# Performance work log

Hardware: AMD Instinct MI355X
Metric: run time of the kernel (lower is better)

Reference implementation:

```python
import jax, jax.numpy as jnp
import numpy as np

B, S, IN, H, NC, WSEG = 2, 256, 80, 128, 40, 64
F2 = 2 * H  # bidirectional LSTM output dim


def setup_inputs() -> dict:
    key = jax.random.key(0)
    it = iter(jax.random.split(key, 48))
    def nrm(shape, scale):
        return jax.random.normal(next(it), shape, jnp.float32) * scale
    d = {}
    d["x"] = jax.random.normal(next(it), (B, S, IN), jnp.float32)
    d["lengths"] = jnp.full((B,), S, dtype=jnp.int32)
    ins = [IN, F2]
    for l in range(2):
        for dr in ("f", "b"):
            sc = 1.0 / np.sqrt(H)
            d[f"w_ih_l{l}{dr}"] = nrm((4 * H, ins[l]), sc)
            d[f"w_hh_l{l}{dr}"] = nrm((4 * H, H), sc)
            d[f"b_l{l}{dr}"] = nrm((4 * H,), sc)
    PD = 3 * F2  # pairwise phi feature dim
    d["a_s0"] = jnp.float32(0.25); d["w_s1"] = nrm((100, PD), 1.0 / np.sqrt(PD)); d["b_s1"] = jnp.zeros((100,), jnp.float32)
    d["a_s1"] = jnp.float32(0.25); d["w_s2"] = nrm((1, 100), 0.1); d["b_s2"] = jnp.zeros((1,), jnp.float32)
    d["a_c0"] = jnp.float32(0.25); d["w_c1"] = nrm((2 * NC, F2), 1.0 / np.sqrt(F2)); d["b_c1"] = jnp.zeros((2 * NC,), jnp.float32)
    d["a_c1"] = jnp.float32(0.25); d["w_c2"] = nrm((NC, 2 * NC), 0.1); d["b_c2"] = jnp.zeros((NC,), jnp.float32)
    d["a_b0"] = jnp.float32(0.25); d["w_b1"] = nrm((2 * NC, F2), 1.0 / np.sqrt(F2)); d["b_b1"] = jnp.zeros((2 * NC,), jnp.float32)
    d["a_b1"] = jnp.float32(0.25); d["w_b2"] = nrm((2, 2 * NC), 0.1); d["b_b2"] = jnp.zeros((2,), jnp.float32)
    return d


def prelu(x, a):
    return jnp.where(x >= 0, x, a * x)


def mlp(x, a0, W1, b1, a1, W2, b2):
    h = prelu(x, a0) @ W1.T + b1
    return prelu(h, a1) @ W2.T + b2


def lstm_dir(x, Wih, Whh, b, reverse):
    # PyTorch gate order: i, f, g, o
    pre = jnp.einsum("bsi,gi->sbg", x, Wih) + b  # [S,B,4H]
    if reverse:
        pre = pre[::-1]
    h0 = jnp.zeros((x.shape[0], Whh.shape[1]), x.dtype)
    def step(carry, xt):
        h, c = carry
        g = xt + h @ Whh.T
        i, f, gg, o = jnp.split(g, 4, axis=-1)
        c = jax.nn.sigmoid(f) * c + jax.nn.sigmoid(i) * jnp.tanh(gg)
        h = jax.nn.sigmoid(o) * jnp.tanh(c)
        return (h, c), h
    _, hs = jax.lax.scan(step, (h0, h0), pre)
    if reverse:
        hs = hs[::-1]
    return jnp.swapaxes(hs, 0, 1)  # [B,S,H]


def encode(x, layers):
    out = x
    for (wif, whf, bf, wib, whb, bb) in layers:
        out = jnp.concatenate([
            lstm_dir(out, wif, whf, bf, False),
            lstm_dir(out, wib, whb, bb, True),
        ], axis=-1)
    return out


def compute_scores(rnn_out, a_s0, w_s1, b_s1, a_s1, w_s2, b_s2):
    cum = jnp.cumsum(rnn_out, axis=1)
    # phi[b,i,j] = [cum[j]-cum[i], out[i], out[j]]  (faithful to calc_phi)
    c = cum[:, None, :, :] - cum[:, :, None, :]
    sh = c.shape
    dmat = jnp.broadcast_to(rnn_out[:, :, None, :], sh)
    emat = jnp.broadcast_to(rnn_out[:, None, :, :], sh)
    phi = jnp.concatenate([c, dmat, emat], axis=-1)  # [B,S,S,3*F2]
    return mlp(phi, a_s0, w_s1, b_s1, a_s1, w_s2, b_s2)[..., 0]  # [B,S,S]


def dp_backptr(scores):
    # Viterbi-style DP: best[i] = max_{j in [i-WSEG, i)} best[j] + scores[:, j, i]
    Bn, Sn = scores.shape[:2]
    def step(best, i):
        start = jnp.maximum(0, i - WSEG)
        jidx = start + jnp.arange(WSEG)
        bwin = jax.lax.dynamic_slice(best, (0, start), (Bn, WSEG))
        swin = jax.lax.dynamic_slice(scores, (0, start, i), (Bn, WSEG, 1))[..., 0]
        cand = jnp.where(jidx[None, :] < i, bwin + swin, -1e9)
        k = (start + jnp.argmax(cand, axis=1)).astype(jnp.int32)
        best = jax.lax.dynamic_update_slice(best, jnp.max(cand, axis=1, keepdims=True), (0, i))
        return best, k
    _, ks = jax.lax.scan(step, jnp.zeros((Bn, Sn), scores.dtype), jnp.arange(1, Sn))
    backptr = jnp.concatenate([jnp.zeros((1, Bn), jnp.int32), ks], axis=0).T  # [B,S]
    return backptr


def backtrack(scores, backptr, lengths):
    Bn, Sn = scores.shape[:2]
    bar = jnp.arange(Bn)
    def step(carry, _):
        cur, acc, bm = carry
        bm = bm.at[bar, cur].set(True)
        prev = backptr[bar, cur]
        active = cur > 0
        acc = acc + jnp.where(active, scores[bar, prev, cur], 0.0)
        cur = jnp.where(active, prev, 0)
        return (cur, acc, bm), None
    init = ((lengths - 1).astype(jnp.int32), jnp.zeros((Bn,), scores.dtype), jnp.zeros((Bn, Sn), bool))
    (_, acc, bm), _ = jax.lax.scan(step, init, None, length=Sn)
    return bm, acc


def reference(x, lengths,
              w_ih_l0f, w_hh_l0f, b_l0f, w_ih_l0b, w_hh_l0b, b_l0b,
              w_ih_l1f, w_hh_l1f, b_l1f, w_ih_l1b, w_hh_l1b, b_l1b,
              a_s0, w_s1, b_s1, a_s1, w_s2, b_s2,
              a_c0, w_c1, b_c1, a_c1, w_c2, b_c2,
              a_b0, w_b1, b_b1, a_b1, w_b2, b_b2):
    layers = [
        (w_ih_l0f, w_hh_l0f, b_l0f, w_ih_l0b, w_hh_l0b, b_l0b),
        (w_ih_l1f, w_hh_l1f, b_l1f, w_ih_l1b, w_hh_l1b, b_l1b),
    ]
    rnn_out = encode(x, layers)  # [B,S,2H]
    cls_out = mlp(rnn_out, a_c0, w_c1, b_c1, a_c1, w_c2, b_c2)
    bin_out = mlp(rnn_out, a_b0, w_b1, b_b1, a_b1, w_b2, b_b2)
    scores = compute_scores(rnn_out, a_s0, w_s1, b_s1, a_s1, w_s2, b_s2)
    backptr = dp_backptr(scores)
    bmask, pred_scores = backtrack(scores, backptr, lengths)
    # bmask[b,i]==1 iff i is a predicted segment boundary (padded-dense encoding of pred lists)
    return cls_out, bin_out, bmask.astype(jnp.int32), pred_scores
```

## Files before the change

### kernel.cpp

```cpp
#include <hip/hip_runtime.h>
#include <math.h>


#define OFF_BIN 20480
#define OFF_BM  21504
#define OFF_PRED 22016

__device__ __forceinline__ float preluf(float x, float a) { return x >= 0.f ? x : a * x; }
__device__ __forceinline__ float sigf(float x) { return 1.f / (1.f + __expf(-x)); }
__device__ __forceinline__ float tanh_fast(float x) { return 1.f - 2.f / (__expf(2.f * x) + 1.f); }

__global__ __launch_bounds__(256) void k_pre2(const float* __restrict__ A,
                                              const float* __restrict__ B,
                                              int Adim, int K,
                                              const float* __restrict__ wf,
                                              const float* __restrict__ bf,
                                              const float* __restrict__ wb,
                                              const float* __restrict__ bb,
                                              float* __restrict__ outF,
                                              float* __restrict__ outB) {
    __shared__ __align__(16) float xs[4 * 256];
    int r0 = blockIdx.x << 2;
    int tid = threadIdx.x;
    int Bdim = K - Adim;
    for (int e = tid; e < 4 * K; e += 256) {
        int row = e / K, kk = e - row * K;
        int tb = r0 + row; int t = tb >> 1, b = tb & 1;
        float v = (kk < Adim) ? A[(size_t)((b << 8) + t) * Adim + kk]
                              : B[(size_t)((b << 8) + t) * Bdim + (kk - Adim)];
        xs[row * K + kk] = v;
    }
    __syncthreads();
    int g = tid;
    const float* w0 = wf + (size_t)g * K;
    const float* w1 = wf + (size_t)(g + 256) * K;
    const float* w2 = wb + (size_t)g * K;
    const float* w3 = wb + (size_t)(g + 256) * K;
    float acc0[4], acc1[4], acc2[4], acc3[4];
    float b0v = bf[g], b1v = bf[g + 256], b2v = bb[g], b3v = bb[g + 256];
#pragma unroll
    for (int r = 0; r < 4; ++r) { acc0[r] = b0v; acc1[r] = b1v; acc2[r] = b2v; acc3[r] = b3v; }
    for (int k = 0; k < K; k += 4) {
        float4 wq0 = *(const float4*)(w0 + k);
        float4 wq1 = *(const float4*)(w1 + k);
        float4 wq2 = *(const float4*)(w2 + k);
        float4 wq3 = *(const float4*)(w3 + k);
#pragma unroll
        for (int r = 0; r < 4; ++r) {
            float4 xq = *(const float4*)(xs + r * K + k);
            acc0[r] += wq0.x * xq.x + wq0.y * xq.y + wq0.z * xq.z + wq0.w * xq.w;
            acc1[r] += wq1.x * xq.x + wq1.y * xq.y + wq1.z * xq.z + wq1.w * xq.w;
            acc2[r] += wq2.x * xq.x + wq2.y * xq.y + wq2.z * xq.z + wq2.w * xq.w;
            acc3[r] += wq3.x * xq.x + wq3.y * xq.y + wq3.z * xq.z + wq3.w * xq.w;
        }
    }
#pragma unroll
    for (int r = 0; r < 4; ++r) {
        int tb = r0 + r;
        outF[(size_t)tb * 512 + g]       = acc0[r];
        outF[(size_t)tb * 512 + 256 + g] = acc1[r];
        outB[(size_t)tb * 512 + g]       = acc2[r];
        outB[(size_t)tb * 512 + 256 + g] = acc3[r];
    }
}

__global__ __launch_bounds__(512, 2) void k_lstm(const float* __restrict__ pre_f,
                                                 const float* __restrict__ pre_b,
                                                 const float* __restrict__ whh_f,
                                                 const float* __restrict__ whh_b,
                                                 float* __restrict__ hout_f,
                                                 float* __restrict__ hout_b) {
    const int dir = blockIdx.x >> 1;
    const int b = blockIdx.x & 1;
    const float* pre = dir ? pre_b : pre_f;
    const float* whh = dir ? whh_b : whh_f;
    float* hout = dir ? hout_b : hout_f;
    const int tid = threadIdx.x;
    const int c = tid >> 7;
    const int gg = tid & 127;
    const int k0 = c << 5;

    float w[4][32];
#pragma unroll
    for (int j = 0; j < 4; ++j) {
#pragma unroll
        for (int k = 0; k < 32; k += 4) {
            float4 v = *(const float4*)(whh + (size_t)((j << 7) + gg) * 128 + k0 + k);
            w[j][k] = v.x; w[j][k + 1] = v.y; w[j][k + 2] = v.z; w[j][k + 3] = v.w;
        }
    }

    __shared__ __align__(16) float hl[128];
    __shared__ float4 part[4][128];
    if (tid < 128) hl[tid] = 0.f;
    float cst = 0.f;
    __syncthreads();

    int t0 = dir ? 255 : 0;
    const float* pp0 = pre + ((size_t)t0 * 2 + b) * 512;
    float p0 = pp0[gg], p1 = pp0[128 + gg], p2 = pp0[256 + gg], p3 = pp0[384 + gg];

    for (int step = 0; step < 256; ++step) {
        int t = dir ? (255 - step) : step;
        float n0 = 0.f, n1 = 0.f, n2 = 0.f, n3 = 0.f;
        if (step < 255) {
            int tn = dir ? (254 - step) : (step + 1);
            const float* pp = pre + ((size_t)tn * 2 + b) * 512;
            n0 = pp[gg]; n1 = pp[128 + gg]; n2 = pp[256 + gg]; n3 = pp[384 + gg];
        }
        float a0 = 0.f, a1 = 0.f, a2 = 0.f, a3 = 0.f;
#pragma unroll
        for (int k = 0; k < 32; k += 4) {
            float4 h4 = *(const float4*)(hl + k0 + k);
            a0 += w[0][k] * h4.x + w[0][k + 1] * h4.y + w[0][k + 2] * h4.z + w[0][k + 3] * h4.w;
            a1 += w[1][k] * h4.x + w[1][k + 1] * h4.y + w[1][k + 2] * h4.z + w[1][k + 3] * h4.w;
            a2 += w[2][k] * h4.x + w[2][k + 1] * h4.y + w[2][k + 2] * h4.z + w[2][k + 3] * h4.w;
            a3 += w[3][k] * h4.x + w[3][k + 1] * h4.y + w[3][k + 2] * h4.z + w[3][k + 3] * h4.w;
        }
        part[c][gg] = make_float4(a0, a1, a2, a3);
        __syncthreads();
        float4 q0 = part[0][gg], q1 = part[1][gg], q2 = part[2][gg], q3 = part[3][gg];
        float gi = p0 + ((q0.x + q1.x) + (q2.x + q3.x));
        float gf = p1 + ((q0.y + q1.y) + (q2.y + q3.y));
        float gG = p2 + ((q0.z + q1.z) + (q2.z + q3.z));
        float go = p3 + ((q0.w + q1.w) + (q2.w + q3.w));
        cst = sigf(gf) * cst + sigf(gi) * tanh_fast(gG);
        float h = sigf(go) * tanh_fast(cst);
        hl[gg] = h;
        if (tid < 128) hout[(size_t)(((b << 8) + t) << 7) + gg] = h;
        p0 = n0; p1 = n1; p2 = n2; p3 = n3;
        __syncthreads();
    }
}

__global__ __launch_bounds__(256) void k_feats(const float* __restrict__ h1f,
                                               const float* __restrict__ h1b,
                                               const float* __restrict__ ws1,
                                               const float* __restrict__ bs1,
                                               const float* a_s0,
                                               float* __restrict__ Pd,
                                               float* __restrict__ Pe,
                                               const float* ac0p, const float* __restrict__ wc1,
                                               const float* __restrict__ bc1, const float* ac1p,
                                               const float* __restrict__ wc2, const float* __restrict__ bc2,
                                               const float* ab0p, const float* __restrict__ wb1,
                                               const float* __restrict__ bb1, const float* ab1p,
                                               const float* __restrict__ wb2, const float* __restrict__ bb2,
                                               float* __restrict__ out,
                                               float* __restrict__ cum) {
    __shared__ __align__(16) float xa[256];
    __shared__ __align__(16) float xb2[256];
    __shared__ __align__(16) float hc[80];
    __shared__ __align__(16) float hb[80];
    int bid = blockIdx.x;
    int tid = threadIdx.x;
    int kk = tid & 127;
    if (bid < 512) {
        int row = bid;
        float a0 = a_s0[0];
        float v = ((tid < 128) ? h1f : h1b)[(size_t)row * 128 + kk];
        xa[tid] = preluf(v, a0);
        __syncthreads();
        const float4* p4 = (const float4*)xa;
        if (tid < 100) {
            const float4* wr = (const float4*)(ws1 + (size_t)tid * 768 + 256);
            float acc = bs1[tid];
#pragma unroll 8
            for (int q = 0; q < 64; ++q) {
                float4 w4 = wr[q], x4 = p4[q];
                acc += w4.x * x4.x + w4.y * x4.y + w4.z * x4.z + w4.w * x4.w;
            }
            Pd[(size_t)row * 100 + tid] = acc;
        } else if (tid >= 128 && tid < 228) {
            int u = tid - 128;
            const float4* wr = (const float4*)(ws1 + (size_t)u * 768 + 512);
            float acc = 0.f;
#pragma unroll 8
            for (int q = 0; q < 64; ++q) {
                float4 w4 = wr[q], x4 = p4[q];
                acc += w4.x * x4.x + w4.y * x4.y + w4.z * x4.z + w4.w * x4.w;
            }
            Pe[(size_t)row * 100 + u] = acc;
        }
    } else if (bid < 1024) {
        int row = bid - 512;
        float ac0 = ac0p[0], ac1 = ac1p[0], ab0 = ab0p[0], ab1 = ab1p[0];
        float v = ((tid < 128) ? h1f : h1b)[(size_t)row * 128 + kk];
        xa[tid] = preluf(v, ac0);
        xb2[tid] = preluf(v, ab0);
        __syncthreads();
        if (tid < 80) {
            const float4* wr = (const float4*)(wc1 + (size_t)tid * 256);
            const float4* x4 = (const float4*)xa;
            float acc = bc1[tid];
#pragma unroll 8
            for (int q = 0; q < 64; ++q) {
                float4 w4 = wr[q], p = x4[q];
                acc += w4.x * p.x + w4.y * p.y + w4.z * p.z + w4.w * p.w;
            }
            hc[tid] = preluf(acc, ac1);
        } else if (tid >= 128 && tid < 208) {
            int u = tid - 128;
            const float4* wr = (const float4*)(wb1 + (size_t)u * 256);
            const float4* x4 = (const float4*)xb2;
            float acc = bb1[u];
#pragma unroll 8
            for (int q = 0; q < 64; ++q) {
                float4 w4 = wr[q], p = x4[q];
                acc += w4.x * p.x + w4.y * p.y + w4.z * p.z + w4.w * p.w;
            }
            hb[u] = preluf(acc, ab1);
        }
        __syncthreads();
        if (tid < 40) {
            const float4* wr = (const float4*)(wc2 + (size_t)tid * 80);
            const float4* h4 = (const float4*)hc;
            float acc = bc2[tid];
#pragma unroll
            for (int q = 0; q < 20; ++q) {
                float4 w4 = wr[q], p = h4[q];
                acc += w4.x * p.x + w4.y * p.y + w4.z * p.z + w4.w * p.w;
            }
            out[(size_t)row * 40 + tid] = acc;
        } else if (tid >= 64 && tid < 66) {
            int j = tid - 64;
            const float4* wr = (const float4*)(wb2 + (size_t)j * 80);
            const float4* h4 = (const float4*)hb;
            float acc = bb2[j];
#pragma unroll
            for (int q = 0; q < 20; ++q) {
                float4 w4 = wr[q], p = h4[q];
                acc += w4.x * p.x + w4.y * p.y + w4.z * p.z + w4.w * p.w;
            }
            out[OFF_BIN + (size_t)row * 2 + j] = acc;
        }
    } else {
        int b = bid - 1024;
        const float* src = (tid < 128) ? h1f : h1b;
        float run = 0.f;
#pragma unroll 8
        for (int t = 0; t < 256; ++t) {
            float v = src[(size_t)(((b << 8) + t) << 7) + kk];
            cum[(size_t)(((b << 8) + t) << 8) + tid] = run + v;
            run += v;
        }
    }
}

__global__ __launch_bounds__(256) void k_scores(const float* __restrict__ cum,
                                                const float* __restrict__ ws1,
                                                const float* __restrict__ ws2,
                                                const float* __restrict__ bs2,
                                                const float* __restrict__ Pd,
                                                const float* __restrict__ Pe,
                                                const float* a_s0p, const float* a_s1p,
                                                float* __restrict__ scT) {
    int bid = blockIdx.x;
    int dt = bid & 3, e = (bid >> 2) & 255, b = bid >> 10;
    int d0 = dt << 6;
    int tid = threadIdx.x;
    __shared__ float cume[256];
    __shared__ float Y[64 * 257];
    __shared__ float red[4][64];
    float a0 = a_s0p[0], a1 = a_s1p[0];
    cume[tid] = cum[(size_t)(((b << 8) + e) << 8) + tid];
    __syncthreads();
#pragma unroll 4
    for (int dj = 0; dj < 64; ++dj) {
        float cd = cum[(size_t)(((b << 8) + (d0 + dj)) << 8) + tid];
        Y[dj * 257 + tid] = preluf(cume[tid] - cd, a0);
    }
    __syncthreads();
    int ug = __builtin_amdgcn_readfirstlane(tid >> 6);
    int ld = tid & 63;
    int d = d0 + ld;
    float acc[25];
#pragma unroll
    for (int t = 0; t < 25; ++t) acc[t] = 0.f;
    const float* wc = ws1 + (size_t)(ug * 25) * 768;
    const float* yrow = Y + ld * 257;
    for (int k = 0; k < 256; k += 4) {
        float y0 = yrow[k], y1 = yrow[k + 1], y2 = yrow[k + 2], y3 = yrow[k + 3];
#pragma unroll
        for (int t = 0; t < 25; ++t) {
            float4 wq = *(const float4*)(wc + (size_t)t * 768 + k);
            acc[t] += y0 * wq.x + y1 * wq.y + y2 * wq.z + y3 * wq.w;
        }
    }
    const float* pdrow = Pd + (size_t)((b << 8) + d) * 100;
    const float* perow = Pe + (size_t)((b << 8) + e) * 100;
    float part = 0.f;
#pragma unroll
    for (int t = 0; t < 25; ++t) {
        int u = ug * 25 + t;
        float h = acc[t] + pdrow[u] + perow[u];
        part += preluf(h, a1) * ws2[u];
    }
    red[ug][ld] = part;
    __syncthreads();
    if (tid < 64) {
        float s = red[0][tid] + red[1][tid] + red[2][tid] + red[3][tid] + bs2[0];
        scT[(size_t)(((b << 8) + e) << 8) + d0 + tid] = s;
    }
}

__global__ __launch_bounds__(128) void k_dp(const float* __restrict__ scT,
                                            const int* __restrict__ lengths,
                                            float* __restrict__ out) {
    __shared__ float best[2][256];
    __shared__ int bp[2][256];
    __shared__ float bm[2][256];
    int tid = threadIdx.x;
    for (int i = tid; i < 512; i += 128) {
        ((float*)best)[i] = 0.f;
        ((int*)bp)[i] = 0;
        ((float*)bm)[i] = 0.f;
    }
    __syncthreads();
    int b = tid >> 6, ln = tid & 63;
    const float* sb = scT + ((size_t)b << 16);
    float sc_next = sb[(1 << 8) + ln];
    for (int i = 1; i < 256; ++i) {
        float sc = sc_next;
        if (i < 255) {
            int i2 = i + 1;
            int st2 = (i2 > 64) ? (i2 - 64) : 0;
            sc_next = sb[(i2 << 8) + st2 + ln];
        }
        int start = (i > 64) ? (i - 64) : 0;
        int j = start + ln;
        float v = -1000000000.0f;
        int ki = j;
        if (j < i) v = best[b][j] + sc;
#pragma unroll
        for (int off = 32; off > 0; off >>= 1) {
            float ov = __shfl_down(v, off);
            int ok = __shfl_down(ki, off);
            if (ov > v || (ov == v && ok < ki)) { v = ov; ki = ok; }
        }
        if (ln == 0) { best[b][i] = v; bp[b][i] = ki; }
    }
    __syncthreads();
    if (tid < 2) {
        int bb = tid;
        int cur = lengths[bb] - 1;
        out[OFF_PRED + bb] = best[bb][cur];
        for (int it = 0; it < 256; ++it) {
            bm[bb][cur] = 1.f;
            int prev = bp[bb][cur];
            cur = (cur > 0) ? prev : 0;
        }
    }
    __syncthreads();
    for (int i = tid; i < 512; i += 128) out[OFF_BM + i] = ((float*)bm)[i];
}

extern "C" void kernel_launch(void* const* d_in, const int* in_sizes, int n_in,
                              void* d_out, int out_size, void* d_ws, size_t ws_size,
                              hipStream_t stream) {
    const float* x     = (const float*)d_in[0];
    const int* lengths = (const int*)d_in[1];
    const float* wih0f = (const float*)d_in[2];
    const float* whh0f = (const float*)d_in[3];
    const float* b0f   = (const float*)d_in[4];
    const float* wih0b = (const float*)d_in[5];
    const float* whh0b = (const float*)d_in[6];
    const float* b0b   = (const float*)d_in[7];
    const float* wih1f = (const float*)d_in[8];
    const float* whh1f = (const float*)d_in[9];
    const float* b1f   = (const float*)d_in[10];
    const float* wih1b = (const float*)d_in[11];
    const float* whh1b = (const float*)d_in[12];
    const float* b1b   = (const float*)d_in[13];
    const float* a_s0  = (const float*)d_in[14];
    const float* w_s1  = (const float*)d_in[15];
    const float* b_s1  = (const float*)d_in[16];
    const float* a_s1  = (const float*)d_in[17];
    const float* w_s2  = (const float*)d_in[18];
    const float* b_s2  = (const float*)d_in[19];
    const float* a_c0  = (const float*)d_in[20];
    const float* w_c1  = (const float*)d_in[21];
    const float* b_c1  = (const float*)d_in[22];
    const float* a_c1  = (const float*)d_in[23];
    const float* w_c2  = (const float*)d_in[24];
    const float* b_c2  = (const float*)d_in[25];
    const float* a_b0  = (const float*)d_in[26];
    const float* w_b1  = (const float*)d_in[27];
    const float* b_b1  = (const float*)d_in[28];
    const float* a_b1  = (const float*)d_in[29];
    const float* w_b2  = (const float*)d_in[30];
    const float* b_b2  = (const float*)d_in[31];

    float* wsf = (float*)d_ws;
    float* preF = wsf;
    float* preB = wsf + 262144;
    float* h0f  = wsf + 524288;
    float* h0b  = wsf + 589824;
    float* h1f  = wsf + 655360;
    float* h1b  = wsf + 720896;
    float* cum  = wsf + 786432;
    float* Pd   = wsf + 917504;
    float* Pe   = wsf + 968704;
    float* scT  = wsf + 1019904;
    float* out  = (float*)d_out;

    k_pre2<<<128, 256, 0, stream>>>(x, x, 80, 80, wih0f, b0f, wih0b, b0b, preF, preB);
    k_lstm<<<4, 512, 0, stream>>>(preF, preB, whh0f, whh0b, h0f, h0b);
    k_pre2<<<128, 256, 0, stream>>>(h0f, h0b, 128, 256, wih1f, b1f, wih1b, b1b, preF, preB);
    k_lstm<<<4, 512, 0, stream>>>(preF, preB, whh1f, whh1b, h1f, h1b);
    k_feats<<<1026, 256, 0, stream>>>(h1f, h1b, w_s1, b_s1, a_s0, Pd, Pe,
                                      a_c0, w_c1, b_c1, a_c1, w_c2, b_c2,
                                      a_b0, w_b1, b_b1, a_b1, w_b2, b_b2, out, cum);
    k_scores<<<2048, 256, 0, stream>>>(cum, w_s1, w_s2, b_s2, Pd, Pe, a_s0, a_s1, scT);
    k_dp<<<1, 128, 0, stream>>>(scT, lengths, out);
}
```

Baseline: 1.053 ms.

## Replace input-projection kernel with 64x64 shared-memory tiled GEMM

Rewrites the LSTM input-projection kernel as a classic tiled GEMM. Each block computes a 64-gate by 64-timestep tile, staging 16-wide K slices of weights and activations in shared memory, and each thread accumulates a 4x4 register block. The old kernel had every thread stream its own weight rows from global memory with little reuse; this version aims to cut that global traffic. It launches 128 blocks over both directions and needs two barriers per K step.

```diff
diff --git a/kernel.cpp b/kernel.cpp
--- a/kernel.cpp
+++ b/kernel.cpp
@@ -10,57 +10,62 @@
 __device__ __forceinline__ float sigf(float x) { return 1.f / (1.f + __expf(-x)); }
 __device__ __forceinline__ float tanh_fast(float x) { return 1.f - 2.f / (__expf(2.f * x) + 1.f); }
 
-__global__ __launch_bounds__(256) void k_pre2(const float* __restrict__ A,
+__global__ __launch_bounds__(256) void k_gemm(const float* __restrict__ A,
                                               const float* __restrict__ B,
                                               int Adim, int K,
                                               const float* __restrict__ wf,
                                               const float* __restrict__ bf,
                                               const float* __restrict__ wb,
-                                              const float* __restrict__ bb,
+                                              const float* __restrict__ bbv,
                                               float* __restrict__ outF,
                                               float* __restrict__ outB) {
-    __shared__ __align__(16) float xs[4 * 256];
-    int r0 = blockIdx.x << 2;
+    int mtile = blockIdx.y;
+    int dir = mtile >> 3;
+    const float* W = dir ? wb : wf;
+    const float* bias = dir ? bbv : bf;
+    float* out = dir ? outB : outF;
+    int g0 = (mtile & 7) << 6;
+    int tb0 = blockIdx.x << 6;
     int tid = threadIdx.x;
     int Bdim = K - Adim;
-    for (int e = tid; e < 4 * K; e += 256) {
-        int row = e / K, kk = e - row * K;
-        int tb = r0 + row; int t = tb >> 1, b = tb & 1;
-        float v = (kk < Adim) ? A[(size_t)((b << 8) + t) * Adim + kk]
-                              : B[(size_t)((b << 8) + t) * Bdim + (kk - Adim)];
-        xs[row * K + kk] = v;
-    }
-    __syncthreads();
-    int g = tid;
-    const float* w0 = wf + (size_t)g * K;
-    const float* w1 = wf + (size_t)(g + 256) * K;
-    const float* w2 = wb + (size_t)g * K;
-    const float* w3 = wb + (size_t)(g + 256) * K;
-    float acc0[4], acc1[4], acc2[4], acc3[4];
-    float b0v = bf[g], b1v = bf[g + 256], b2v = bb[g], b3v = bb[g + 256];
-#pragma unroll
-    for (int r = 0; r < 4; ++r) { acc0[r] = b0v; acc1[r] = b1v; acc2[r] = b2v; acc3[r] = b3v; }
-    for (int k = 0; k < K; k += 4) {
-        float4 wq0 = *(const float4*)(w0 + k);
-        float4 wq1 = *(const float4*)(w1 + k);
-        float4 wq2 = *(const float4*)(w2 + k);
-        float4 wq3 = *(const float4*)(w3 + k);
-#pragma unroll
-        for (int r = 0; r < 4; ++r) {
-            float4 xq = *(const float4*)(xs + r * K + k);
-            acc0[r] += wq0.x * xq.x + wq0.y * xq.y + wq0.z * xq.z + wq0.w * xq.w;
-            acc1[r] += wq1.x * xq.x + wq1.y * xq.y + wq1.z * xq.z + wq1.w * xq.w;
-            acc2[r] += wq2.x * xq.x + wq2.y * xq.y + wq2.z * xq.z + wq2.w * xq.w;
-            acc3[r] += wq3.x * xq.x + wq3.y * xq.y + wq3.z * xq.z + wq3.w * xq.w;
-        }
-    }
-#pragma unroll
-    for (int r = 0; r < 4; ++r) {
-        int tb = r0 + r;
-        outF[(size_t)tb * 512 + g]       = acc0[r];
-        outF[(size_t)tb * 512 + 256 + g] = acc1[r];
-        outB[(size_t)tb * 512 + g]       = acc2[r];
-        outB[(size_t)tb * 512 + 256 + g] = acc3[r];
+
+    __shared__ float Ws[16][68];
+    __shared__ float Xs[16][68];
+
+    int r = tid >> 2, c4 = tid & 3;
+    int tbr = tb0 + r;
+    int hr = ((tbr & 1) << 8) | (tbr >> 1);
+    int ty = tid >> 4;
+    int tx = tid & 15;
+    float acc[4][4] = {};
+
+    for (int k0 = 0; k0 < K; k0 += 16) {
+        float4 wv = *(const float4*)(W + (size_t)(g0 + r) * K + k0 + (c4 << 2));
+        const float* src = (k0 < Adim) ? (A + (size_t)hr * Adim + k0)
+                                       : (B + (size_t)hr * Bdim + (k0 - Adim));
+        float4 xv = *(const float4*)(src + (c4 << 2));
+        __syncthreads();
+        int kc = c4 << 2;
+        Ws[kc + 0][r] = wv.x; Ws[kc + 1][r] = wv.y; Ws[kc + 2][r] = wv.z; Ws[kc + 3][r] = wv.w;
+        Xs[kc + 0][r] = xv.x; Xs[kc + 1][r] = xv.y; Xs[kc + 2][r] = xv.z; Xs[kc + 3][r] = xv.w;
+        __syncthreads();
+#pragma unroll
+        for (int kk = 0; kk < 16; ++kk) {
+            float4 wq = *(const float4*)&Ws[kk][ty << 2];
+            float4 xq = *(const float4*)&Xs[kk][tx << 2];
+            acc[0][0] += wq.x * xq.x; acc[0][1] += wq.x * xq.y; acc[0][2] += wq.x * xq.z; acc[0][3] += wq.x * xq.w;
+            acc[1][0] += wq.y * xq.x; acc[1][1] += wq.y * xq.y; acc[1][2] += wq.y * xq.z; acc[1][3] += wq.y * xq.w;
+            acc[2][0] += wq.z * xq.x; acc[2][1] += wq.z * xq.y; acc[2][2] += wq.z * xq.z; acc[2][3] += wq.z * xq.w;
+            acc[3][0] += wq.w * xq.x; acc[3][1] += wq.w * xq.y; acc[3][2] += wq.w * xq.z; acc[3][3] += wq.w * xq.w;
+        }
+    }
+    int gq = g0 + (ty << 2);
+    float b0 = bias[gq], b1 = bias[gq + 1], b2 = bias[gq + 2], b3 = bias[gq + 3];
+#pragma unroll
+    for (int j = 0; j < 4; ++j) {
+        int tb = tb0 + (tx << 2) + j;
+        float4 v = make_float4(acc[0][j] + b0, acc[1][j] + b1, acc[2][j] + b2, acc[3][j] + b3);
+        *(float4*)(out + (size_t)tb * 512 + gq) = v;
     }
 }
 
@@ -404,9 +409,9 @@
     float* scT  = wsf + 1019904;
     float* out  = (float*)d_out;
 
-    k_pre2<<<128, 256, 0, stream>>>(x, x, 80, 80, wih0f, b0f, wih0b, b0b, preF, preB);
+    k_gemm<<<dim3(8, 16), 256, 0, stream>>>(x, x, 80, 80, wih0f, b0f, wih0b, b0b, preF, preB);
     k_lstm<<<4, 512, 0, stream>>>(preF, preB, whh0f, whh0b, h0f, h0b);
-    k_pre2<<<128, 256, 0, stream>>>(h0f, h0b, 128, 256, wih1f, b1f, wih1b, b1b, preF, preB);
+    k_gemm<<<dim3(8, 16), 256, 0, stream>>>(h0f, h0b, 128, 256, wih1f, b1f, wih1b, b1b, preF, preB);
     k_lstm<<<4, 512, 0, stream>>>(preF, preB, whh1f, whh1b, h1f, h1b);
     k_feats<<<1026, 256, 0, stream>>>(h1f, h1b, w_s1, b_s1, a_s0, Pd, Pe,
                                       a_c0, w_c1, b_c1, a_c1, w_c2, b_c2,
```

Result: faster. 1.025 ms (-2.7%).
